# Kernel tuning notes

Measured on AMD Instinct MI355X. Metric: run time of the kernel, lower is better.

## Reference

```python
import math
import jax, jax.numpy as jnp
import numpy as np

LOW_FREQ = 1
FACTOR = 1


def setup_inputs() -> dict:
    key = jax.random.key(0)
    x = jax.random.normal(key, (16, 4096, 256), dtype=jnp.float32)
    return {"x": x}


def reference(x):
    b, t, d = x.shape
    x_freq = jnp.fft.rfft(x, axis=1)  # (b, t//2+1, d) complex
    if t % 2 == 0:
        x_freq = x_freq[:, LOW_FREQ:-1]
        f = jnp.fft.rfftfreq(t)[LOW_FREQ:-1]
    else:
        x_freq = x_freq[:, LOW_FREQ:]
        f = jnp.fft.rfftfreq(t)[LOW_FREQ:]
    f = f.astype(jnp.float32)
    F = x_freq.shape[1]
    top_k = int(FACTOR * math.log(F))  # static (shape-derived)

    # top-k by magnitude along freq axis, independently per (b, d)
    xf_bdf = jnp.moveaxis(x_freq, 1, 2)              # (b, d, F)
    _, idx = jax.lax.top_k(jnp.abs(xf_bdf), top_k)   # (b, d, k) int32
    xf_sel = jnp.take_along_axis(xf_bdf, idx, axis=2)  # (b, d, k)
    xf_sel = jnp.moveaxis(xf_sel, 2, 1)              # (b, k, d)
    f_sel = jnp.moveaxis(f[idx], 2, 1)[:, :, None, :]  # (b, k, 1, d)

    # extrapolate: conj-pair frequencies, synthesize cosines, reduce over freq
    xf2 = jnp.concatenate([xf_sel, jnp.conj(xf_sel)], axis=1)  # (b, 2k, d)
    f2 = jnp.concatenate([f_sel, -f_sel], axis=1)              # (b, 2k, 1, d)
    tt = jnp.arange(t, dtype=jnp.float32)[None, None, :, None]  # (1,1,t,1)
    amp = (jnp.abs(xf2) * 2.0 / t)[:, :, None, :]   # (b, 2k, 1, d)
    phase = jnp.angle(xf2)[:, :, None, :]           # (b, 2k, 1, d)
    x_time = amp * jnp.cos(2.0 * math.pi * f2 * tt + phase)  # (b, 2k, t, d)
    return x_time.sum(axis=1)  # (b, t, d)
```

## Files before the change

kernel.cpp:

```cpp
#include <hip/hip_runtime.h>
#include <math.h>

#define T_LEN 4096
#define N2    2048
#define TOPK  7
#define NCH   256
#define R8F 0.70710678f

#define AD(a) ((a) + ((a) >> 3) + ((a) >> 8))

__global__ __launch_bounds__(256) void prep_kernel(
    const float* __restrict__ x, float* __restrict__ xt,
    double2* __restrict__ tw, float2* __restrict__ twf)
{
    if (blockIdx.x < 16) {
        int p = blockIdx.x * 256 + threadIdx.x;
        double th = -2.0 * 3.14159265358979323846 * (double)p / (double)T_LEN;
        double c = cos(th), s = sin(th);
        tw[p]  = make_double2(c, s);
        twf[p] = make_float2((float)c, (float)s);
        return;
    }
    __shared__ float tile[64][65];
    const int bid = blockIdx.x - 16;
    const int t0  = (bid & 63) * 64;
    const int c0  = ((bid >> 6) & 3) * 64;
    const int b   = bid >> 8;
    const int tx4 = (threadIdx.x & 15) * 4;
    const int ty  = threadIdx.x >> 4;

    const float* src = x + (size_t)b * T_LEN * NCH;
    for (int r = 0; r < 4; ++r) {
        int t = ty + r * 16;
        float4 v = *(const float4*)(src + (size_t)(t0 + t) * NCH + c0 + tx4);
        tile[t][tx4 + 0] = v.x; tile[t][tx4 + 1] = v.y;
        tile[t][tx4 + 2] = v.z; tile[t][tx4 + 3] = v.w;
    }
    __syncthreads();
    float* dst = xt + (size_t)b * NCH * T_LEN;
    for (int r = 0; r < 4; ++r) {
        int c = ty + r * 16;
        float4 v = make_float4(tile[tx4 + 0][c], tile[tx4 + 1][c],
                               tile[tx4 + 2][c], tile[tx4 + 3][c]);
        *(float4*)(dst + (size_t)(c0 + c) * T_LEN + t0 + tx4) = v;
    }
}

__device__ __forceinline__ void dft8_twf(float ar[8], float ai[8],
                                         int base, const float2* __restrict__ twf)
{
    float t0r=ar[0]+ar[4], t0i=ai[0]+ai[4], t4r=ar[0]-ar[4], t4i=ai[0]-ai[4];
    float t1r=ar[1]+ar[5], t1i=ai[1]+ai[5], t5r=ar[1]-ar[5], t5i=ai[1]-ai[5];
    float t2r=ar[2]+ar[6], t2i=ai[2]+ai[6], t6r=ar[2]-ar[6], t6i=ai[2]-ai[6];
    float t3r=ar[3]+ar[7], t3i=ai[3]+ai[7], t7r=ar[3]-ar[7], t7i=ai[3]-ai[7];
    float s0r=t0r+t2r, s0i=t0i+t2i, s2r=t0r-t2r, s2i=t0i-t2i;
    float s1r=t1r+t3r, s1i=t1i+t3i, s3r=t1r-t3r, s3i=t1i-t3i;
    ar[0]=s0r+s1r; ai[0]=s0i+s1i;
    ar[4]=s0r-s1r; ai[4]=s0i-s1i;
    ar[2]=s2r+s3i; ai[2]=s2i-s3r;
    ar[6]=s2r-s3i; ai[6]=s2i+s3r;
    float c1r=R8F*(t5r+t5i), c1i=R8F*(t5i-t5r);
    float c2r=t6i,           c2i=-t6r;
    float c3r=R8F*(t7i-t7r), c3i=-R8F*(t7r+t7i);
    float d0r=t4r+c2r, d0i=t4i+c2i, d1r=t4r-c2r, d1i=t4i-c2i;
    float d2r=c1r+c3r, d2i=c1i+c3i, d3r=c1r-c3r, d3i=c1i-c3i;
    ar[1]=d0r+d2r; ai[1]=d0i+d2i;
    ar[5]=d0r-d2r; ai[5]=d0i-d2i;
    ar[3]=d1r+d3i; ai[3]=d1i-d3r;
    ar[7]=d1r-d3i; ai[7]=d1i+d3r;
#pragma unroll
    for (int m = 1; m < 8; ++m) {
        float2 w = twf[(base * m) & 4095];
        float xr = ar[m], xi = ai[m];
        ar[m] = w.x * xr - w.y * xi;
        ai[m] = w.x * xi + w.y * xr;
    }
}

__device__ __forceinline__ unsigned long long packkey32(float mag, int k) {
    return ((unsigned long long)__float_as_uint(mag) << 32)
         | (unsigned long long)(2047 - k);
}

__global__ __launch_bounds__(256, 8) void fft_topk_kernel(
    const float* __restrict__ xt, const double2* __restrict__ tw,
    const float2* __restrict__ twf,
    int* __restrict__ k_out, float4* __restrict__ ab4)
{
    __shared__ float2 zz[AD(N2 - 1) + 3];
    __shared__ unsigned long long wavetop[4 * TOPK];
    __shared__ unsigned long long selkey[TOPK];

    const int tid = threadIdx.x;
    const int bc  = blockIdx.x;
    const float2* xcol2 = (const float2*)(xt + (size_t)bc * T_LEN);

    float ar[8], ai[8];
#pragma unroll
    for (int u = 0; u < 8; ++u) {
        float2 v = xcol2[tid + (u << 8)];
        ar[u] = v.x; ai[u] = v.y;
    }
    dft8_twf(ar, ai, 2 * tid, twf);
#pragma unroll
    for (int m = 0; m < 8; ++m)
        zz[AD((m << 8) + tid)] = make_float2(ar[m], ai[m]);
    __syncthreads();

    {
        const int g = tid >> 5, j2 = tid & 31, base = (g << 8) + j2;
#pragma unroll
        for (int u = 0; u < 8; ++u) {
            float2 v = zz[AD(base + (u << 5))];
            ar[u] = v.x; ai[u] = v.y;
        }
        dft8_twf(ar, ai, 16 * j2, twf);
#pragma unroll
        for (int m = 0; m < 8; ++m)
            zz[AD(base + (m << 5))] = make_float2(ar[m], ai[m]);
    }
    __syncthreads();

    {
        const int g3 = tid >> 2, j3 = tid & 3, base = (g3 << 5) + j3;
#pragma unroll
        for (int u = 0; u < 8; ++u) {
            float2 v = zz[AD(base + (u << 2))];
            ar[u] = v.x; ai[u] = v.y;
        }
        dft8_twf(ar, ai, 128 * j3, twf);
#pragma unroll
        for (int m = 0; m < 8; ++m)
            zz[AD(base + (m << 2))] = make_float2(ar[m], ai[m]);
    }
    __syncthreads();

#pragma unroll
    for (int q = 0; q < 2; ++q) {
        int h4 = ((q << 8) + tid) << 2;
#pragma unroll
        for (int r = 0; r < 4; ++r) {
            float2 v = zz[AD(h4 + r)];
            ar[q * 4 + r] = v.x; ai[q * 4 + r] = v.y;
        }
    }
    __syncthreads();
#pragma unroll
    for (int q = 0; q < 2; ++q) {
        float b0r = ar[q*4+0], b0i = ai[q*4+0], b1r = ar[q*4+1], b1i = ai[q*4+1];
        float b2r = ar[q*4+2], b2i = ai[q*4+2], b3r = ar[q*4+3], b3i = ai[q*4+3];
        float e0r = b0r + b2r, e0i = b0i + b2i, e1r = b0r - b2r, e1i = b0i - b2i;
        float e2r = b1r + b3r, e2i = b1i + b3i, e3r = b1r - b3r, e3i = b1i - b3i;
        int kbase = ((tid & 7) << 6) | (((tid >> 3) & 7) << 3) | (q << 2) | (tid >> 6);
        zz[AD(kbase)]        = make_float2(e0r + e2r, e0i + e2i);
        zz[AD(kbase + 1024)] = make_float2(e0r - e2r, e0i - e2i);
        zz[AD(kbase +  512)] = make_float2(e1r + e3i, e1i - e3r);
        zz[AD(kbase + 1536)] = make_float2(e1r - e3i, e1i + e3r);
    }
    __syncthreads();

    unsigned long long keys[8];
#pragma unroll
    for (int j = 0; j < 4; ++j) {
        int k  = 1 + tid + (j << 8);
        int kp = N2 - k;
        float2 yk = zz[AD(k)];
        float2 yp = zz[AD(kp)];
        float Ar = 0.5f * (yk.x + yp.x), Ai = 0.5f * (yk.y - yp.y);
        float Br = 0.5f * (yk.y + yp.y), Bi = -0.5f * (yk.x - yp.x);
        float2 t = twf[k];
        float Cr = t.x * Br - t.y * Bi;
        float Ci = t.x * Bi + t.y * Br;
        float m1 = (Ar + Cr) * (Ar + Cr) + (Ai + Ci) * (Ai + Ci);
        float m2 = (Ar - Cr) * (Ar - Cr) + (Ai - Ci) * (Ai - Ci);
        keys[2 * j]     = packkey32(m1, k);
        keys[2 * j + 1] = (kp != k) ? packkey32(m2, kp) : 0ULL;
    }

    const int wv = tid >> 6, ln = tid & 63;
    unsigned long long lb = 0ULL;
#pragma unroll
    for (int s = 0; s < 8; ++s) lb = (keys[s] > lb) ? keys[s] : lb;

    for (int it = 0; it < TOPK; ++it) {
        unsigned long long v = lb;
#pragma unroll
        for (int off = 32; off; off >>= 1) {
            unsigned long long o = __shfl_xor(v, off);
            if (o > v) v = o;
        }
        if (ln == 0) wavetop[wv * TOPK + it] = v;
#pragma unroll
        for (int s = 0; s < 8; ++s) keys[s] = (keys[s] == v) ? 0ULL : keys[s];
        lb = 0ULL;
#pragma unroll
        for (int s = 0; s < 8; ++s) lb = (keys[s] > lb) ? keys[s] : lb;
    }
    __syncthreads();

    if (tid < 32) {
        unsigned long long v = (tid < 4 * TOPK) ? wavetop[tid] : 0ULL;
        for (int it = 0; it < TOPK; ++it) {
            unsigned long long m = v;
#pragma unroll
            for (int off = 16; off; off >>= 1) {
                unsigned long long o = __shfl_xor(m, off);
                if (o > m) m = o;
            }
            if (tid == 0) selkey[it] = m;
            if (m == v) v = 0ULL;
        }
    }
    __syncthreads();

    if (tid < TOPK) {
        int k  = 2047 - (int)(selkey[tid] & 2047ULL);
        float2 ykf = zz[AD(k)];
        float2 ypf = zz[AD(N2 - k)];
        double ykx = (double)ykf.x, yky = (double)ykf.y;
        double ypx = (double)ypf.x, ypy = (double)ypf.y;
        double Ar = 0.5 * (ykx + ypx), Ai = 0.5 * (yky - ypy);
        double Br = 0.5 * (yky + ypy), Bi = -0.5 * (ykx - ypx);
        double2 t = tw[k];
        double Xr = Ar + t.x * Br - t.y * Bi;
        double Xi = Ai + t.x * Bi + t.y * Br;
        k_out[tid * 4096 + bc] = k;
        ab4[tid * 4096 + bc] = make_float4(
            (float)( 4.0 * Xr / (double)T_LEN),
            (float)(-4.0 * Xi / (double)T_LEN),
            (float)t.x, (float)(-t.y));
    }
}

__global__ __launch_bounds__(256) void recon_kernel(
    const int* __restrict__ k_in, const float4* __restrict__ ab4,
    float* __restrict__ out)
{
    __shared__ float tile[16][256];

    const int tid   = threadIdx.x;
    const int chunk = blockIdx.x & 127;
    const int b     = blockIdx.x >> 7;
    const int bc    = (b << 8) + tid;
    const int n0    = chunk << 5;

    const float c0 = 6.28318530717958647692f / 4096.0f;
    float aa[TOPK], bb[TOPK], zr[TOPK], zi[TOPK], wr[TOPK], wi[TOPK];
#pragma unroll
    for (int j = 0; j < TOPK; ++j) {
        int k    = k_in[j * 4096 + bc];
        float4 v = ab4[j * 4096 + bc];
        aa[j] = v.x; bb[j] = v.y; wr[j] = v.z; wi[j] = v.w;
        int m0 = (k * n0) & (T_LEN - 1);
        float ang = (float)m0 * c0;
        zr[j] = __cosf(ang);
        zi[j] = __sinf(ang);
    }

    float* obase = out + ((size_t)b * T_LEN + n0) * NCH;
    for (int r = 0; r < 2; ++r) {
#pragma unroll
        for (int i = 0; i < 16; ++i) {
            float acc = 0.f;
#pragma unroll
            for (int j = 0; j < TOPK; ++j) {
                acc += aa[j] * zr[j] + bb[j] * zi[j];
                float nzr = zr[j] * wr[j] - zi[j] * wi[j];
                zi[j] = zr[j] * wi[j] + zi[j] * wr[j];
                zr[j] = nzr;
            }
            tile[i][tid] = acc;
        }
        __syncthreads();
#pragma unroll
        for (int s = 0; s < 4; ++s) {
            int fid = tid + (s << 8);
            int ni  = fid >> 6;
            int c4  = (fid & 63) << 2;
            float4 v = make_float4(tile[ni][c4], tile[ni][c4 + 1],
                                   tile[ni][c4 + 2], tile[ni][c4 + 3]);
            *(float4*)(obase + (size_t)((r << 4) + ni) * NCH + c4) = v;
        }
        __syncthreads();
    }
}

extern "C" void kernel_launch(void* const* d_in, const int* in_sizes, int n_in,
                              void* d_out, int out_size, void* d_ws, size_t ws_size,
                              hipStream_t stream) {
    const float* x   = (const float*)d_in[0];
    float*       out = (float*)d_out;
    char*        ws  = (char*)d_ws;

    double2* tw    = (double2*)(ws);
    int*     k_ws  = (int*)   (ws + 65536);
    float4*  ab_ws = (float4*)(ws + 180224);
    float2*  twf   = (float2*)(ws + 638976);

    prep_kernel     <<<16 + 4096, 256, 0, stream>>>(x, out, tw, twf);
    fft_topk_kernel <<<4096, 256, 0, stream>>>(out, tw, twf, k_ws, ab_ws);
    recon_kernel    <<<2048, 256, 0, stream>>>(k_ws, ab_ws, out);
}
```

Before: 186.8 us.

## Compute FFT twiddle powers in registers, sort keys for top-k, use nontemporal IO

Each radix-8 stage now loads one twiddle and derives powers 2 through 7 by complex multiplication, replacing seven table loads. The per-thread keys are presorted with a sorting network so each top-k round pops the head instead of rescanning all eight. The wave max is now reduced on the 32-bit magnitude first, with a ballot fast path. Input loads and output stores become nontemporal and recon uses sincos. Deriving twiddles by repeated multiplication can add rounding error.

```diff
diff --git a/kernel.cpp b/kernel.cpp
--- a/kernel.cpp
+++ b/kernel.cpp
@@ -8,6 +8,19 @@
 #define R8F 0.70710678f
 
 #define AD(a) ((a) + ((a) >> 3) + ((a) >> 8))
+
+typedef float nt_f4 __attribute__((ext_vector_type(4)));
+
+typedef float2 c32;
+__device__ __forceinline__ c32 cadd(c32 a, c32 b) { return make_float2(a.x + b.x, a.y + b.y); }
+__device__ __forceinline__ c32 csub(c32 a, c32 b) { return make_float2(a.x - b.x, a.y - b.y); }
+__device__ __forceinline__ c32 cmul(c32 a, c32 w) {
+    return make_float2(w.x * a.x - w.y * a.y, w.x * a.y + w.y * a.x);
+}
+__device__ __forceinline__ c32 csq(c32 a) {
+    return make_float2(a.x * a.x - a.y * a.y, 2.0f * a.x * a.y);
+}
+__device__ __forceinline__ c32 mulnegi(c32 a) { return make_float2(a.y, -a.x); }
 
 __global__ __launch_bounds__(256) void prep_kernel(
     const float* __restrict__ x, float* __restrict__ xt,
@@ -32,7 +45,8 @@
     const float* src = x + (size_t)b * T_LEN * NCH;
     for (int r = 0; r < 4; ++r) {
         int t = ty + r * 16;
-        float4 v = *(const float4*)(src + (size_t)(t0 + t) * NCH + c0 + tx4);
+        nt_f4 v = __builtin_nontemporal_load(
+            (const nt_f4*)(src + (size_t)(t0 + t) * NCH + c0 + tx4));
         tile[t][tx4 + 0] = v.x; tile[t][tx4 + 1] = v.y;
         tile[t][tx4 + 2] = v.z; tile[t][tx4 + 3] = v.w;
     }
@@ -46,41 +60,52 @@
     }
 }
 
-__device__ __forceinline__ void dft8_twf(float ar[8], float ai[8],
-                                         int base, const float2* __restrict__ twf)
+__device__ __forceinline__ void dft8_pw(c32 x[8], c32 w1)
 {
-    float t0r=ar[0]+ar[4], t0i=ai[0]+ai[4], t4r=ar[0]-ar[4], t4i=ai[0]-ai[4];
-    float t1r=ar[1]+ar[5], t1i=ai[1]+ai[5], t5r=ar[1]-ar[5], t5i=ai[1]-ai[5];
-    float t2r=ar[2]+ar[6], t2i=ai[2]+ai[6], t6r=ar[2]-ar[6], t6i=ai[2]-ai[6];
-    float t3r=ar[3]+ar[7], t3i=ai[3]+ai[7], t7r=ar[3]-ar[7], t7i=ai[3]-ai[7];
-    float s0r=t0r+t2r, s0i=t0i+t2i, s2r=t0r-t2r, s2i=t0i-t2i;
-    float s1r=t1r+t3r, s1i=t1i+t3i, s3r=t1r-t3r, s3i=t1i-t3i;
-    ar[0]=s0r+s1r; ai[0]=s0i+s1i;
-    ar[4]=s0r-s1r; ai[4]=s0i-s1i;
-    ar[2]=s2r+s3i; ai[2]=s2i-s3r;
-    ar[6]=s2r-s3i; ai[6]=s2i+s3r;
-    float c1r=R8F*(t5r+t5i), c1i=R8F*(t5i-t5r);
-    float c2r=t6i,           c2i=-t6r;
-    float c3r=R8F*(t7i-t7r), c3i=-R8F*(t7r+t7i);
-    float d0r=t4r+c2r, d0i=t4i+c2i, d1r=t4r-c2r, d1i=t4i-c2i;
-    float d2r=c1r+c3r, d2i=c1i+c3i, d3r=c1r-c3r, d3i=c1i-c3i;
-    ar[1]=d0r+d2r; ai[1]=d0i+d2i;
-    ar[5]=d0r-d2r; ai[5]=d0i-d2i;
-    ar[3]=d1r+d3i; ai[3]=d1i-d3r;
-    ar[7]=d1r-d3i; ai[7]=d1i+d3r;
-#pragma unroll
-    for (int m = 1; m < 8; ++m) {
-        float2 w = twf[(base * m) & 4095];
-        float xr = ar[m], xi = ai[m];
-        ar[m] = w.x * xr - w.y * xi;
-        ai[m] = w.x * xi + w.y * xr;
-    }
+    c32 t0 = cadd(x[0], x[4]), t4 = csub(x[0], x[4]);
+    c32 t1 = cadd(x[1], x[5]), t5 = csub(x[1], x[5]);
+    c32 t2 = cadd(x[2], x[6]), t6 = csub(x[2], x[6]);
+    c32 t3 = cadd(x[3], x[7]), t7 = csub(x[3], x[7]);
+    c32 s0 = cadd(t0, t2), s2 = csub(t0, t2);
+    c32 s1 = cadd(t1, t3), s3 = csub(t1, t3);
+    x[0] = cadd(s0, s1);
+    x[4] = csub(s0, s1);
+    c32 s3n = mulnegi(s3);
+    x[2] = cadd(s2, s3n);
+    x[6] = csub(s2, s3n);
+    c32 c1 = make_float2(R8F * (t5.x + t5.y), R8F * (t5.y - t5.x));
+    c32 c2 = mulnegi(t6);
+    c32 c3 = make_float2(R8F * (t7.y - t7.x), -R8F * (t7.x + t7.y));
+    c32 d0 = cadd(t4, c2), d1 = csub(t4, c2);
+    c32 d2 = cadd(c1, c3), d3 = csub(c1, c3);
+    x[1] = cadd(d0, d2);
+    x[5] = csub(d0, d2);
+    c32 d3n = mulnegi(d3);
+    x[3] = cadd(d1, d3n);
+    x[7] = csub(d1, d3n);
+
+    c32 w2 = csq(w1);
+    c32 w3 = cmul(w1, w2);
+    c32 w4 = csq(w2);
+    c32 w5 = cmul(w3, w2);
+    c32 w6 = csq(w3);
+    c32 w7 = cmul(w4, w3);
+    x[1] = cmul(x[1], w1);
+    x[2] = cmul(x[2], w2);
+    x[3] = cmul(x[3], w3);
+    x[4] = cmul(x[4], w4);
+    x[5] = cmul(x[5], w5);
+    x[6] = cmul(x[6], w6);
+    x[7] = cmul(x[7], w7);
 }
 
 __device__ __forceinline__ unsigned long long packkey32(float mag, int k) {
     return ((unsigned long long)__float_as_uint(mag) << 32)
          | (unsigned long long)(2047 - k);
 }
+
+#define CSWAP(i, j) { unsigned long long a_ = keys[i], b_ = keys[j]; \
+                      keys[i] = a_ > b_ ? a_ : b_; keys[j] = a_ > b_ ? b_ : a_; }
 
 __global__ __launch_bounds__(256, 8) void fft_topk_kernel(
     const float* __restrict__ xt, const double2* __restrict__ tw,
@@ -95,43 +120,37 @@
     const int bc  = blockIdx.x;
     const float2* xcol2 = (const float2*)(xt + (size_t)bc * T_LEN);
 
-    float ar[8], ai[8];
-#pragma unroll
-    for (int u = 0; u < 8; ++u) {
-        float2 v = xcol2[tid + (u << 8)];
-        ar[u] = v.x; ai[u] = v.y;
-    }
-    dft8_twf(ar, ai, 2 * tid, twf);
+    c32 x[8];
+#pragma unroll
+    for (int u = 0; u < 8; ++u)
+        x[u] = xcol2[tid + (u << 8)];
+    dft8_pw(x, twf[2 * tid]);
 #pragma unroll
     for (int m = 0; m < 8; ++m)
-        zz[AD((m << 8) + tid)] = make_float2(ar[m], ai[m]);
+        zz[AD((m << 8) + tid)] = x[m];
     __syncthreads();
 
     {
         const int g = tid >> 5, j2 = tid & 31, base = (g << 8) + j2;
 #pragma unroll
-        for (int u = 0; u < 8; ++u) {
-            float2 v = zz[AD(base + (u << 5))];
-            ar[u] = v.x; ai[u] = v.y;
-        }
-        dft8_twf(ar, ai, 16 * j2, twf);
+        for (int u = 0; u < 8; ++u)
+            x[u] = zz[AD(base + (u << 5))];
+        dft8_pw(x, twf[16 * j2]);
 #pragma unroll
         for (int m = 0; m < 8; ++m)
-            zz[AD(base + (m << 5))] = make_float2(ar[m], ai[m]);
+            zz[AD(base + (m << 5))] = x[m];
     }
     __syncthreads();
 
     {
         const int g3 = tid >> 2, j3 = tid & 3, base = (g3 << 5) + j3;
 #pragma unroll
-        for (int u = 0; u < 8; ++u) {
-            float2 v = zz[AD(base + (u << 2))];
-            ar[u] = v.x; ai[u] = v.y;
-        }
-        dft8_twf(ar, ai, 128 * j3, twf);
+        for (int u = 0; u < 8; ++u)
+            x[u] = zz[AD(base + (u << 2))];
+        dft8_pw(x, twf[128 * j3]);
 #pragma unroll
         for (int m = 0; m < 8; ++m)
-            zz[AD(base + (m << 2))] = make_float2(ar[m], ai[m]);
+            zz[AD(base + (m << 2))] = x[m];
     }
     __syncthreads();
 
@@ -139,23 +158,21 @@
     for (int q = 0; q < 2; ++q) {
         int h4 = ((q << 8) + tid) << 2;
 #pragma unroll
-        for (int r = 0; r < 4; ++r) {
-            float2 v = zz[AD(h4 + r)];
-            ar[q * 4 + r] = v.x; ai[q * 4 + r] = v.y;
-        }
+        for (int r = 0; r < 4; ++r)
+            x[q * 4 + r] = zz[AD(h4 + r)];
     }
     __syncthreads();
 #pragma unroll
     for (int q = 0; q < 2; ++q) {
-        float b0r = ar[q*4+0], b0i = ai[q*4+0], b1r = ar[q*4+1], b1i = ai[q*4+1];
-        float b2r = ar[q*4+2], b2i = ai[q*4+2], b3r = ar[q*4+3], b3i = ai[q*4+3];
-        float e0r = b0r + b2r, e0i = b0i + b2i, e1r = b0r - b2r, e1i = b0i - b2i;
-        float e2r = b1r + b3r, e2i = b1i + b3i, e3r = b1r - b3r, e3i = b1i - b3i;
+        c32 b0 = x[q*4+0], b1 = x[q*4+1], b2 = x[q*4+2], b3 = x[q*4+3];
+        c32 e0 = cadd(b0, b2), e1 = csub(b0, b2);
+        c32 e2 = cadd(b1, b3), e3 = csub(b1, b3);
+        c32 e3n = mulnegi(e3);
         int kbase = ((tid & 7) << 6) | (((tid >> 3) & 7) << 3) | (q << 2) | (tid >> 6);
-        zz[AD(kbase)]        = make_float2(e0r + e2r, e0i + e2i);
-        zz[AD(kbase + 1024)] = make_float2(e0r - e2r, e0i - e2i);
-        zz[AD(kbase +  512)] = make_float2(e1r + e3i, e1i - e3r);
-        zz[AD(kbase + 1536)] = make_float2(e1r - e3i, e1i + e3r);
+        zz[AD(kbase)]        = cadd(e0, e2);
+        zz[AD(kbase + 1024)] = csub(e0, e2);
+        zz[AD(kbase +  512)] = cadd(e1, e3n);
+        zz[AD(kbase + 1536)] = csub(e1, e3n);
     }
     __syncthreads();
 
@@ -177,24 +194,45 @@
         keys[2 * j + 1] = (kp != k) ? packkey32(m2, kp) : 0ULL;
     }
 
+    CSWAP(0,1) CSWAP(2,3) CSWAP(4,5) CSWAP(6,7)
+    CSWAP(0,2) CSWAP(1,3) CSWAP(4,6) CSWAP(5,7)
+    CSWAP(1,2) CSWAP(5,6)
+    CSWAP(0,4) CSWAP(1,5) CSWAP(2,6) CSWAP(3,7)
+    CSWAP(2,4) CSWAP(3,5)
+    CSWAP(1,2) CSWAP(3,4) CSWAP(5,6)
+
     const int wv = tid >> 6, ln = tid & 63;
-    unsigned long long lb = 0ULL;
-#pragma unroll
-    for (int s = 0; s < 8; ++s) lb = (keys[s] > lb) ? keys[s] : lb;
+    unsigned long long lb = keys[0];
 
     for (int it = 0; it < TOPK; ++it) {
-        unsigned long long v = lb;
+        unsigned int hl = (unsigned int)(lb >> 32);
+        unsigned int h  = hl;
 #pragma unroll
         for (int off = 32; off; off >>= 1) {
-            unsigned long long o = __shfl_xor(v, off);
-            if (o > v) v = o;
+            unsigned int o = __shfl_xor(h, off);
+            h = (o > h) ? o : h;
+        }
+        unsigned long long mask = __ballot(hl == h);
+        unsigned long long v;
+        if (__popcll(mask) == 1) {
+            int src = __ffsll((long long)mask) - 1;
+            v = ((unsigned long long)h << 32)
+              | (unsigned long long)__shfl((unsigned int)lb, src);
+        } else {
+            unsigned int l = (hl == h) ? (unsigned int)lb : 0u;
+#pragma unroll
+            for (int off = 32; off; off >>= 1) {
+                unsigned int o = __shfl_xor(l, off);
+                l = (o > l) ? o : l;
+            }
+            v = ((unsigned long long)h << 32) | l;
         }
         if (ln == 0) wavetop[wv * TOPK + it] = v;
-#pragma unroll
-        for (int s = 0; s < 8; ++s) keys[s] = (keys[s] == v) ? 0ULL : keys[s];
-        lb = 0ULL;
-#pragma unroll
-        for (int s = 0; s < 8; ++s) lb = (keys[s] > lb) ? keys[s] : lb;
+        if (v == lb && v) {
+            keys[0]=keys[1]; keys[1]=keys[2]; keys[2]=keys[3]; keys[3]=keys[4];
+            keys[4]=keys[5]; keys[5]=keys[6]; keys[6]=keys[7]; keys[7]=0ULL;
+            lb = keys[0];
+        }
     }
     __syncthreads();
 
@@ -245,16 +283,16 @@
     const int n0    = chunk << 5;
 
     const float c0 = 6.28318530717958647692f / 4096.0f;
-    float aa[TOPK], bb[TOPK], zr[TOPK], zi[TOPK], wr[TOPK], wi[TOPK];
+    float aa[TOPK], bb[TOPK];
+    c32 z[TOPK], w[TOPK];
 #pragma unroll
     for (int j = 0; j < TOPK; ++j) {
         int k    = k_in[j * 4096 + bc];
         float4 v = ab4[j * 4096 + bc];
-        aa[j] = v.x; bb[j] = v.y; wr[j] = v.z; wi[j] = v.w;
+        aa[j] = v.x; bb[j] = v.y; w[j] = make_float2(v.z, v.w);
         int m0 = (k * n0) & (T_LEN - 1);
         float ang = (float)m0 * c0;
-        zr[j] = __cosf(ang);
-        zi[j] = __sinf(ang);
+        __sincosf(ang, &z[j].y, &z[j].x);
     }
 
     float* obase = out + ((size_t)b * T_LEN + n0) * NCH;
@@ -264,10 +302,8 @@
             float acc = 0.f;
 #pragma unroll
             for (int j = 0; j < TOPK; ++j) {
-                acc += aa[j] * zr[j] + bb[j] * zi[j];
-                float nzr = zr[j] * wr[j] - zi[j] * wi[j];
-                zi[j] = zr[j] * wi[j] + zi[j] * wr[j];
-                zr[j] = nzr;
+                acc += aa[j] * z[j].x + bb[j] * z[j].y;
+                z[j] = cmul(z[j], w[j]);
             }
             tile[i][tid] = acc;
         }
@@ -277,9 +313,10 @@
             int fid = tid + (s << 8);
             int ni  = fid >> 6;
             int c4  = (fid & 63) << 2;
-            float4 v = make_float4(tile[ni][c4], tile[ni][c4 + 1],
-                                   tile[ni][c4 + 2], tile[ni][c4 + 3]);
-            *(float4*)(obase + (size_t)((r << 4) + ni) * NCH + c4) = v;
+            nt_f4 v = { tile[ni][c4], tile[ni][c4 + 1],
+                        tile[ni][c4 + 2], tile[ni][c4 + 3] };
+            __builtin_nontemporal_store(v,
+                (nt_f4*)(obase + (size_t)((r << 4) + ni) * NCH + c4));
         }
         __syncthreads();
     }
```

New measurement: 172.7 us. -7.5%, faster.
